# Kernel tuning notes

Hardware: AMD Instinct MI355X
Metric: run time of the kernel (lower is better)

Reference implementation:

```python
import math
import jax, jax.numpy as jnp
import numpy as np

LLM = 4096
QB = 512
SAM = 256
H = W = 64
OUT = 256
HEADS = 4
DH = SAM // HEADS
EPS = 1e-5


def _ln(x, g, b):
    mu = jnp.mean(x, axis=-1, keepdims=True)
    var = jnp.mean(jnp.square(x - mu), axis=-1, keepdims=True)
    return (x - mu) * jax.lax.rsqrt(var + EPS) * g + b


def _conv3x3(x, w):
    # x: (N,C,H,W), w: (O,I,3,3), padding=1
    return jax.lax.conv_general_dilated(
        x, w, window_strides=(1, 1), padding='SAME',
        dimension_numbers=('NCHW', 'OIHW', 'NCHW'))


def setup_inputs() -> dict:
    key = jax.random.key(0)
    ks = jax.random.split(key, 20)
    n = lambda k, sh, s: (jax.random.normal(k, sh, dtype=jnp.float32) * s)
    inp = {
        'image_embed': n(ks[0], (8, SAM, H, W), 1.0),
        'ref_vec': n(ks[1], (8, 32, LLM), 1.0),
        'querybook_slots': n(ks[2], (8, 32, QB), 1.0),
        # parameters (torch Linear layout: (out, in); conv: (O,I,kh,kw))
        'q_proj_w': n(ks[3], (HEADS * DH, LLM), 1.0 / math.sqrt(LLM)),
        'k_proj_w': n(ks[4], (HEADS * DH, SAM, 1, 1), 1.0 / math.sqrt(SAM)),
        'fuser_w1': n(ks[5], (HEADS, HEADS, 3, 3), 1.0 / math.sqrt(HEADS * 9)),
        'fuser_b1': n(ks[6], (HEADS,), 0.01),
        'fuser_w2': n(ks[7], (1, HEADS, 3, 3), 1.0 / math.sqrt(HEADS * 9)),
        'fuser_b2': jnp.full((1,), -1.8, dtype=jnp.float32),
        'qb_proj_w': n(ks[8], (LLM, QB), 1.0 / math.sqrt(QB)),
        'rf_ln_g': jnp.ones((2 * LLM,), jnp.float32),
        'rf_ln_b': jnp.zeros((2 * LLM,), jnp.float32),
        'rf_lin_w': n(ks[9], (LLM, 2 * LLM), 1.0 / math.sqrt(2 * LLM)),
        'rf_lin_b': n(ks[10], (LLM,), 0.01),
        'cf_ln_g': jnp.ones((LLM,), jnp.float32),
        'cf_ln_b': jnp.zeros((LLM,), jnp.float32),
        'cf_w1': n(ks[11], (LLM // 2, LLM), 1.0 / math.sqrt(LLM)),
        'cf_b1': n(ks[12], (LLM // 2,), 0.01),
        'cf_w2': n(ks[13], (1, LLM // 2), 1.0 / math.sqrt(LLM // 2)),
        'cf_b2': n(ks[14], (1,), 0.01),
    }
    return inp


def reference(image_embed, ref_vec, querybook_slots, q_proj_w, k_proj_w,
              fuser_w1, fuser_b1, fuser_w2, fuser_b2, qb_proj_w,
              rf_ln_g, rf_ln_b, rf_lin_w, rf_lin_b,
              cf_ln_g, cf_ln_b, cf_w1, cf_b1, cf_w2, cf_b2):
    B, C, h, w = image_embed.shape
    K = ref_vec.shape[1]
    # querybook projection + ref fuse
    qb = jnp.einsum('bkq,lq->bkl', querybook_slots, qb_proj_w)  # (B,K,LLM)
    cat = jnp.concatenate([ref_vec, qb], axis=-1)               # (B,K,2*LLM)
    fused = jax.nn.silu(jnp.einsum('bkc,lc->bkl', _ln(cat, rf_ln_g, rf_ln_b), rf_lin_w) + rf_lin_b)
    # per-slot query heads
    Q = jnp.einsum('bkl,ol->bko', fused, q_proj_w).reshape(B, K, HEADS, DH)
    # 1x1 conv key map -> (B,HEADS,DH,H,W)
    Kmap = jnp.einsum('bcxy,oc->boxy', image_embed, k_proj_w.reshape(HEADS * DH, SAM))
    Kmap = Kmap.reshape(B, HEADS, DH, h, w)
    # fused contraction over d_head (original materialized (B,K,HEADS,DH,H,W))
    logits_64_heads = jnp.einsum('bkhd,bhdxy->bkhxy', Q, Kmap) / math.sqrt(DH)
    x = logits_64_heads.reshape(B * K, HEADS, h, w)
    x = jax.nn.silu(_conv3x3(x, fuser_w1) + fuser_b1[None, :, None, None])
    logits_64 = _conv3x3(x, fuser_w2) + fuser_b2[None, :, None, None]  # (B*K,1,64,64)
    # bilinear upsample, align_corners=False (half-pixel centers)
    up = jax.image.resize(logits_64, (B * K, 1, OUT, OUT), method='bilinear')
    ref_logits_256 = up.reshape(B, K, OUT, OUT)
    # confidence head
    cfh = jax.nn.silu(jnp.einsum('bkl,ol->bko', _ln(fused, cf_ln_g, cf_ln_b), cf_w1) + cf_b1)
    conf_logits = (jnp.einsum('bko,lo->bkl', cfh, cf_w2) + cf_b2).squeeze(-1)  # (B,K)
    return ref_logits_256, conf_logits
```

## Files before the change

### kernel.cpp

```cpp
#include <hip/hip_runtime.h>

#define EPS 1e-5f

typedef __bf16 bf16_t;
typedef __bf16 bf16x8 __attribute__((ext_vector_type(8)));
typedef __bf16 bf16x4 __attribute__((ext_vector_type(4)));
typedef float f32x4 __attribute__((ext_vector_type(4)));

__device__ __forceinline__ float silu_f(float x) { return x / (1.f + __expf(-x)); }

__device__ __forceinline__ float block_sum(float v, float* tmp) {
#pragma unroll
  for (int off = 32; off > 0; off >>= 1) v += __shfl_down(v, off);
  __syncthreads();
  if ((threadIdx.x & 63) == 0) tmp[threadIdx.x >> 6] = v;
  __syncthreads();
  return tmp[0] + tmp[1] + tmp[2] + tmp[3];
}

__global__ __launch_bounds__(1024) void gemm_wide(
    const bf16_t* __restrict__ A, const float* __restrict__ B,
    bf16_t* __restrict__ Cpart, int N, int K, int KS) {
  __shared__ bf16_t As[2][256][72];
  __shared__ bf16_t Bs[2][128][72];
  const int t = threadIdx.x;
  const int lane = t & 63;
  const int w = t >> 6;
  const int n0 = blockIdx.x * 128;
  const int kbeg = blockIdx.y * KS;
  const int nt = KS >> 6;
  const int ar = t >> 2, ac = (t & 3) * 16;
  const int br = t >> 3, bc = (t & 7) * 8;
  const bf16_t* Ap = A + (size_t)ar * K + kbeg + ac;
  const float* Bp = B + (size_t)(n0 + br) * K + kbeg + bc;

  bf16x8 a0X, a1X, a0Y, a1Y, a0Z, a1Z;
  float4 b0X, b1X, b0Y, b1Y, b0Z, b1Z;

#define LOADSET(S, k0)                            \
  a0##S = *(const bf16x8*)(Ap + (k0));            \
  a1##S = *(const bf16x8*)(Ap + (k0) + 8);        \
  b0##S = *(const float4*)(Bp + (k0));            \
  b1##S = *(const float4*)(Bp + (k0) + 4);

#define STORESET(S, buf)                                                    \
  {                                                                         \
    *(bf16x8*)&As[buf][ar][ac] = a0##S;                                     \
    *(bf16x8*)&As[buf][ar][ac + 8] = a1##S;                                 \
    bf16x8 wv;                                                              \
    wv[0] = (bf16_t)b0##S.x; wv[1] = (bf16_t)b0##S.y;                       \
    wv[2] = (bf16_t)b0##S.z; wv[3] = (bf16_t)b0##S.w;                       \
    wv[4] = (bf16_t)b1##S.x; wv[5] = (bf16_t)b1##S.y;                       \
    wv[6] = (bf16_t)b1##S.z; wv[7] = (bf16_t)b1##S.w;                       \
    *(bf16x8*)&Bs[buf][br][bc] = wv;                                        \
  }

  f32x4 acc[4][2];
#pragma unroll
  for (int i = 0; i < 4; ++i)
#pragma unroll
    for (int j = 0; j < 2; ++j) acc[i][j] = f32x4{0.f, 0.f, 0.f, 0.f};

  const int wm = (w & 3) * 64;
  const int wn = (w >> 2) * 32;
  const int fr = lane & 15;
  const int kq = (lane >> 4) * 8;

  auto COMPUTE = [&](int buf) {
#pragma unroll
    for (int kk = 0; kk < 64; kk += 32) {
      bf16x8 af[4], bg[2];
#pragma unroll
      for (int i = 0; i < 4; ++i)
        af[i] = *(const bf16x8*)&As[buf][wm + 16 * i + fr][kk + kq];
#pragma unroll
      for (int j = 0; j < 2; ++j)
        bg[j] = *(const bf16x8*)&Bs[buf][wn + 16 * j + fr][kk + kq];
#pragma unroll
      for (int i = 0; i < 4; ++i)
#pragma unroll
        for (int j = 0; j < 2; ++j)
          acc[i][j] = __builtin_amdgcn_mfma_f32_16x16x32_bf16(af[i], bg[j], acc[i][j], 0, 0, 0);
    }
  };

#define SB __builtin_amdgcn_sched_barrier(0);
#define END_PHASE                                      \
  asm volatile("s_waitcnt lgkmcnt(0)" ::: "memory");   \
  SB __builtin_amdgcn_s_barrier(); SB

#define PHASE(s_, LS, SS, bufc)                              \
  if ((s_) < nt) {                                           \
    if ((s_) + 3 < nt) { LOADSET(LS, ((s_) + 3) * 64) }      \
    SB                                                       \
    if ((s_) + 1 < nt) { STORESET(SS, bufc ^ 1) }            \
    COMPUTE(bufc);                                           \
    END_PHASE                                                \
  }

  LOADSET(X, 0)
  if (1 < nt) { LOADSET(Y, 64) }
  if (2 < nt) { LOADSET(Z, 128) }
  SB
  STORESET(X, 0)
  END_PHASE

  for (int s6 = 0; s6 < nt; s6 += 6) {
    PHASE(s6 + 0, X, Y, 0)
    PHASE(s6 + 1, Y, Z, 1)
    PHASE(s6 + 2, Z, X, 0)
    PHASE(s6 + 3, X, Y, 1)
    PHASE(s6 + 4, Y, Z, 0)
    PHASE(s6 + 5, Z, X, 1)
  }
#undef LOADSET
#undef STORESET
#undef PHASE
#undef END_PHASE
#undef SB

  bf16_t* Cz = Cpart + (size_t)blockIdx.y * 256 * N;
  const int rh = (lane >> 4) * 4, col = lane & 15;
#pragma unroll
  for (int i = 0; i < 4; ++i)
#pragma unroll
    for (int j = 0; j < 2; ++j)
#pragma unroll
      for (int rr = 0; rr < 4; ++rr)
        Cz[(size_t)(wm + 16 * i + rh + rr) * N + n0 + wn + 16 * j + col] =
            (bf16_t)acc[i][j][rr];
}

__global__ __launch_bounds__(1024) void gemm_wide_s(
    const float* __restrict__ A, const float* __restrict__ B,
    bf16_t* __restrict__ Cpart, int N, int K, int KS) {
  __shared__ bf16_t As[256][72];
  __shared__ bf16_t Bs[128][72];
  const int t = threadIdx.x;
  const int lane = t & 63;
  const int w = t >> 6;
  const int n0 = blockIdx.x * 128;
  const int kbeg = blockIdx.y * KS;
  const int nt = KS >> 6;
  const int ar = t >> 2, ac = (t & 3) * 16;
  const int br = t >> 3, bc = (t & 7) * 8;
  const float* Ap = A + (size_t)ar * K + kbeg + ac;
  const float* Bp = B + (size_t)(n0 + br) * K + kbeg + bc;

  f32x4 acc[4][2];
#pragma unroll
  for (int i = 0; i < 4; ++i)
#pragma unroll
    for (int j = 0; j < 2; ++j) acc[i][j] = f32x4{0.f, 0.f, 0.f, 0.f};

  const int wm = (w & 3) * 64;
  const int wn = (w >> 2) * 32;
  const int fr = lane & 15;
  const int kq = (lane >> 4) * 8;

  for (int s = 0; s < nt; ++s) {
    float4 av[4], bv[2];
#pragma unroll
    for (int i = 0; i < 4; ++i) av[i] = *(const float4*)(Ap + s * 64 + 4 * i);
#pragma unroll
    for (int i = 0; i < 2; ++i) bv[i] = *(const float4*)(Bp + s * 64 + 4 * i);
    __syncthreads();
    {
      bf16x8 wa0, wa1, wb;
      wa0[0] = (bf16_t)av[0].x; wa0[1] = (bf16_t)av[0].y; wa0[2] = (bf16_t)av[0].z; wa0[3] = (bf16_t)av[0].w;
      wa0[4] = (bf16_t)av[1].x; wa0[5] = (bf16_t)av[1].y; wa0[6] = (bf16_t)av[1].z; wa0[7] = (bf16_t)av[1].w;
      wa1[0] = (bf16_t)av[2].x; wa1[1] = (bf16_t)av[2].y; wa1[2] = (bf16_t)av[2].z; wa1[3] = (bf16_t)av[2].w;
      wa1[4] = (bf16_t)av[3].x; wa1[5] = (bf16_t)av[3].y; wa1[6] = (bf16_t)av[3].z; wa1[7] = (bf16_t)av[3].w;
      wb[0] = (bf16_t)bv[0].x; wb[1] = (bf16_t)bv[0].y; wb[2] = (bf16_t)bv[0].z; wb[3] = (bf16_t)bv[0].w;
      wb[4] = (bf16_t)bv[1].x; wb[5] = (bf16_t)bv[1].y; wb[6] = (bf16_t)bv[1].z; wb[7] = (bf16_t)bv[1].w;
      *(bf16x8*)&As[ar][ac] = wa0;
      *(bf16x8*)&As[ar][ac + 8] = wa1;
      *(bf16x8*)&Bs[br][bc] = wb;
    }
    __syncthreads();
#pragma unroll
    for (int kk = 0; kk < 64; kk += 32) {
      bf16x8 af[4], bg[2];
#pragma unroll
      for (int i = 0; i < 4; ++i)
        af[i] = *(const bf16x8*)&As[wm + 16 * i + fr][kk + kq];
#pragma unroll
      for (int j = 0; j < 2; ++j)
        bg[j] = *(const bf16x8*)&Bs[wn + 16 * j + fr][kk + kq];
#pragma unroll
      for (int i = 0; i < 4; ++i)
#pragma unroll
        for (int j = 0; j < 2; ++j)
          acc[i][j] = __builtin_amdgcn_mfma_f32_16x16x32_bf16(af[i], bg[j], acc[i][j], 0, 0, 0);
    }
    __syncthreads();
  }

  bf16_t* Cz = Cpart + (size_t)blockIdx.y * 256 * N;
  const int rh = (lane >> 4) * 4, col = lane & 15;
#pragma unroll
  for (int i = 0; i < 4; ++i)
#pragma unroll
    for (int j = 0; j < 2; ++j)
#pragma unroll
      for (int rr = 0; rr < 4; ++rr)
        Cz[(size_t)(wm + 16 * i + rh + rr) * N + n0 + wn + 16 * j + col] =
            (bf16_t)acc[i][j][rr];
}

__global__ __launch_bounds__(256) void gemm_small(
    const bf16_t* __restrict__ A16, const float* __restrict__ B32, float* __restrict__ Cv,
    int M, int N, int K, int KS, int S) {
  __shared__ bf16_t As[64][72];
  __shared__ bf16_t Bs[64][72];
  const int t = threadIdx.x;
  const int lane = t & 63;
  const int w = t >> 6;
  const int s = blockIdx.z;
  const int n0 = blockIdx.x * 64;
  const int m0 = blockIdx.y * 64;
  const int kbeg = s * KS;

  f32x4 acc[2][2];
#pragma unroll
  for (int i = 0; i < 2; ++i)
#pragma unroll
    for (int j = 0; j < 2; ++j) acc[i][j] = f32x4{0.f, 0.f, 0.f, 0.f};

  const int wm = (w & 1) * 32, wn = (w >> 1) * 32;
  const int fr = lane & 15;
  const int kq = (lane >> 4) * 8;

  for (int k0 = kbeg; k0 < kbeg + KS; k0 += 64) {
    bf16x8 a8[2];
    float4 b4[4];
    {
      const int rr = t >> 2, c8 = (t & 3) * 8;
#pragma unroll
      for (int i = 0; i < 2; ++i)
        a8[i] = *(const bf16x8*)(A16 + (size_t)(m0 + rr) * K + k0 + c8 + 32 * i);
    }
    {
      const int rr = t >> 4, c4 = (t & 15) * 4;
#pragma unroll
      for (int i = 0; i < 4; ++i)
        b4[i] = *(const float4*)(B32 + (size_t)(n0 + rr + 16 * i) * K + k0 + c4);
    }
    __syncthreads();
    {
      const int rr = t >> 2, c8 = (t & 3) * 8;
#pragma unroll
      for (int i = 0; i < 2; ++i) *(bf16x8*)&As[rr][c8 + 32 * i] = a8[i];
    }
    {
      const int rr = t >> 4, c4 = (t & 15) * 4;
#pragma unroll
      for (int i = 0; i < 4; ++i) {
        bf16x4 v = {(bf16_t)b4[i].x, (bf16_t)b4[i].y, (bf16_t)b4[i].z, (bf16_t)b4[i].w};
        *(bf16x4*)&Bs[rr + 16 * i][c4] = v;
      }
    }
    __syncthreads();
#pragma unroll
    for (int kk = 0; kk < 64; kk += 32) {
      bf16x8 af[2], bg[2];
#pragma unroll
      for (int i = 0; i < 2; ++i) {
        af[i] = *(const bf16x8*)&As[wm + 16 * i + fr][kk + kq];
        bg[i] = *(const bf16x8*)&Bs[wn + 16 * i + fr][kk + kq];
      }
#pragma unroll
      for (int i = 0; i < 2; ++i)
#pragma unroll
        for (int j = 0; j < 2; ++j)
          acc[i][j] = __builtin_amdgcn_mfma_f32_16x16x32_bf16(af[i], bg[j], acc[i][j], 0, 0, 0);
    }
    __syncthreads();
  }

  const int rh = (lane >> 4) * 4;
  const int col = lane & 15;
#pragma unroll
  for (int i = 0; i < 2; ++i)
#pragma unroll
    for (int j = 0; j < 2; ++j)
#pragma unroll
      for (int rr = 0; rr < 4; ++rr)
        Cv[(size_t)s * M * N + (size_t)(m0 + wm + 16 * i + rh + rr) * N + n0 + wn + 16 * j + col] =
            acc[i][j][rr];
}

__global__ __launch_bounds__(512) void gemm_attn(
    const float* __restrict__ A, const float* __restrict__ B, bf16_t* __restrict__ C) {
  __shared__ bf16_t As[128][72];
  __shared__ bf16_t Bs[64][72];
  const int t = threadIdx.x;
  const int lane = t & 63;
  const int w = t >> 6;
  const int b = blockIdx.y;
  const int n0 = blockIdx.x * 64;
  const float* Ab = A + (size_t)b * 32768;
  const float* Bb = B + (size_t)b * 1048576;

  f32x4 acc[2][2];
#pragma unroll
  for (int i = 0; i < 2; ++i)
#pragma unroll
    for (int j = 0; j < 2; ++j) acc[i][j] = f32x4{0.f, 0.f, 0.f, 0.f};

  const int wm = (w & 3) * 32;
  const int wn = (w >> 2) * 32;
  const int fr = lane & 15;
  const int kq = (lane >> 4) * 8;

  for (int k0 = 0; k0 < 256; k0 += 64) {
    const int r = t >> 2, c4 = (t & 3) * 16;
    float4 a4[4];
#pragma unroll
    for (int i = 0; i < 4; ++i)
      a4[i] = *(const float4*)(Ab + (size_t)r * 256 + k0 + c4 + 4 * i);
    const int kr = t >> 3, nc = (t & 7) * 8;
    float4 b4[2];
#pragma unroll
    for (int i = 0; i < 2; ++i)
      b4[i] = *(const float4*)(Bb + (size_t)(k0 + kr) * 4096 + n0 + nc + 4 * i);
    __syncthreads();
#pragma unroll
    for (int i = 0; i < 4; ++i) {
      bf16x4 v = {(bf16_t)a4[i].x, (bf16_t)a4[i].y, (bf16_t)a4[i].z, (bf16_t)a4[i].w};
      *(bf16x4*)&As[r][c4 + 4 * i] = v;
    }
#pragma unroll
    for (int i = 0; i < 2; ++i) {
      Bs[nc + 4 * i + 0][kr] = (bf16_t)b4[i].x;
      Bs[nc + 4 * i + 1][kr] = (bf16_t)b4[i].y;
      Bs[nc + 4 * i + 2][kr] = (bf16_t)b4[i].z;
      Bs[nc + 4 * i + 3][kr] = (bf16_t)b4[i].w;
    }
    __syncthreads();
#pragma unroll
    for (int kk = 0; kk < 64; kk += 32) {
      bf16x8 af[2], bg[2];
#pragma unroll
      for (int i = 0; i < 2; ++i) {
        af[i] = *(const bf16x8*)&As[wm + 16 * i + fr][kk + kq];
        bg[i] = *(const bf16x8*)&Bs[wn + 16 * i + fr][kk + kq];
      }
#pragma unroll
      for (int i = 0; i < 2; ++i)
#pragma unroll
        for (int j = 0; j < 2; ++j)
          acc[i][j] = __builtin_amdgcn_mfma_f32_16x16x32_bf16(af[i], bg[j], acc[i][j], 0, 0, 0);
    }
    __syncthreads();
  }

  bf16_t* Cb = C + (size_t)b * 524288;
  const int rh = (lane >> 4) * 4, col = lane & 15;
#pragma unroll
  for (int i = 0; i < 2; ++i)
#pragma unroll
    for (int j = 0; j < 2; ++j)
#pragma unroll
      for (int rr = 0; rr < 4; ++rr)
        Cb[(size_t)(wm + 16 * i + rh + rr) * 4096 + n0 + wn + 16 * j + col] =
            (bf16_t)acc[i][j][rr];
}

template <int SILU_, int BIAS_>
__global__ __launch_bounds__(256) void reduce_b(
    const bf16_t* __restrict__ part, int S, long slice,
    const float* __restrict__ bias, float scale,
    float* __restrict__ outF, bf16_t* __restrict__ outB,
    long nmask, long total8) {
  long i8 = (long)blockIdx.x * 256 + threadIdx.x;
  if (i8 >= total8) return;
  long i = i8 * 8;
  float a[8] = {0.f, 0.f, 0.f, 0.f, 0.f, 0.f, 0.f, 0.f};
  for (int s = 0; s < S; ++s) {
    bf16x8 v = *(const bf16x8*)(part + (size_t)s * slice + i);
#pragma unroll
    for (int j = 0; j < 8; ++j) a[j] += (float)v[j];
  }
#pragma unroll
  for (int j = 0; j < 8; ++j) a[j] *= scale;
  if (BIAS_) {
    const float* bb = bias + (i & nmask);
#pragma unroll
    for (int j = 0; j < 8; ++j) a[j] += bb[j];
  }
  if (SILU_) {
#pragma unroll
    for (int j = 0; j < 8; ++j) a[j] = silu_f(a[j]);
  }
  if (outF) {
    float4 o0 = {a[0], a[1], a[2], a[3]}, o1 = {a[4], a[5], a[6], a[7]};
    *(float4*)(outF + i) = o0;
    *(float4*)(outF + i + 4) = o1;
  }
  if (outB) {
    bf16x8 o;
#pragma unroll
    for (int j = 0; j < 8; ++j) o[j] = (bf16_t)a[j];
    *(bf16x8*)(outB + i) = o;
  }
}

__global__ __launch_bounds__(256) void ln_fuse(
    const float* __restrict__ refv, const bf16_t* __restrict__ partQ, int S,
    const float* __restrict__ g, const float* __restrict__ bta, bf16_t* __restrict__ Y) {
  __shared__ float tmp[4];
  const int row = blockIdx.x;
  const int t = threadIdx.x;
  const long i0 = t * 16;
  float q[16];
#pragma unroll
  for (int j = 0; j < 16; ++j) q[j] = 0.f;
  for (int s = 0; s < S; ++s) {
    const bf16_t* p = partQ + (size_t)s * 1048576 + (size_t)row * 4096 + i0;
    bf16x8 v0 = *(const bf16x8*)(p);
    bf16x8 v1 = *(const bf16x8*)(p + 8);
#pragma unroll
    for (int j = 0; j < 8; ++j) { q[j] += (float)v0[j]; q[8 + j] += (float)v1[j]; }
  }
  const float* xr = refv + (size_t)row * 4096 + i0;
  float r[16];
#pragma unroll
  for (int j = 0; j < 4; ++j) {
    float4 v = *(const float4*)(xr + 4 * j);
    r[4 * j] = v.x; r[4 * j + 1] = v.y; r[4 * j + 2] = v.z; r[4 * j + 3] = v.w;
  }
  float s1 = 0.f, s2 = 0.f;
#pragma unroll
  for (int j = 0; j < 16; ++j) { s1 += r[j] + q[j]; s2 += r[j] * r[j] + q[j] * q[j]; }
  s1 = block_sum(s1, tmp);
  s2 = block_sum(s2, tmp);
  const float mu = s1 / 8192.f;
  const float inv = rsqrtf(s2 / 8192.f - mu * mu + EPS);
  bf16_t* y = Y + (size_t)row * 8192;
  bf16x8 o0, o1;
#pragma unroll
  for (int j = 0; j < 8; ++j) {
    o0[j] = (bf16_t)((r[j] - mu) * inv * g[i0 + j] + bta[i0 + j]);
    o1[j] = (bf16_t)((r[8 + j] - mu) * inv * g[i0 + 8 + j] + bta[i0 + 8 + j]);
  }
  *(bf16x8*)(y + i0) = o0;
  *(bf16x8*)(y + i0 + 8) = o1;
#pragma unroll
  for (int j = 0; j < 8; ++j) {
    o0[j] = (bf16_t)((q[j] - mu) * inv * g[4096 + i0 + j] + bta[4096 + i0 + j]);
    o1[j] = (bf16_t)((q[8 + j] - mu) * inv * g[4096 + i0 + 8 + j] + bta[4096 + i0 + 8 + j]);
  }
  *(bf16x8*)(y + 4096 + i0) = o0;
  *(bf16x8*)(y + 4096 + i0 + 8) = o1;
}

__global__ __launch_bounds__(256) void ln_rows(
    const float* __restrict__ X1, int L1,
    const float* __restrict__ g, const float* __restrict__ bta, bf16_t* __restrict__ Y) {
  __shared__ float tmp[4];
  const int row = blockIdx.x;
  const float* x1 = X1 + (size_t)row * L1;
  float s = 0.f, ss = 0.f;
  for (int i = threadIdx.x * 4; i < L1; i += 1024) {
    float4 v = *(const float4*)(x1 + i);
    s += v.x + v.y + v.z + v.w;
    ss += v.x * v.x + v.y * v.y + v.z * v.z + v.w * v.w;
  }
  s = block_sum(s, tmp);
  ss = block_sum(ss, tmp);
  const float mu = s / (float)L1;
  const float inv = rsqrtf(ss / (float)L1 - mu * mu + EPS);
  bf16_t* y = Y + (size_t)row * L1;
  for (int i = threadIdx.x * 4; i < L1; i += 1024) {
    float4 v = *(const float4*)(x1 + i);
    float4 gv = *(const float4*)(g + i);
    float4 bv = *(const float4*)(bta + i);
    bf16x4 o = {(bf16_t)((v.x - mu) * inv * gv.x + bv.x),
                (bf16_t)((v.y - mu) * inv * gv.y + bv.y),
                (bf16_t)((v.z - mu) * inv * gv.z + bv.z),
                (bf16_t)((v.w - mu) * inv * gv.w + bv.w)};
    *(bf16x4*)(y + i) = o;
  }
}

__global__ __launch_bounds__(256) void qw_fuse(
    const float* __restrict__ part8, const float* __restrict__ kW, float* __restrict__ QW) {
  __shared__ float q[256];
  const int bk = blockIdx.x;
  const int c = threadIdx.x;
  float sq = 0.f;
#pragma unroll
  for (int s = 0; s < 8; ++s) sq += part8[(size_t)s * 65536 + (size_t)bk * 256 + c];
  q[c] = 0.125f * sq;
  __syncthreads();
#pragma unroll
  for (int h = 0; h < 4; ++h) {
    float s = 0.f;
#pragma unroll 8
    for (int d = 0; d < 64; ++d)
      s += q[(h << 6) + d] * kW[(size_t)(((h << 6) + d) << 8) + c];
    QW[((size_t)(bk * 4 + h) << 8) + c] = s;
  }
}

__global__ __launch_bounds__(256) void conv_fused(
    const bf16_t* __restrict__ X, const float* __restrict__ W1,
    const float* __restrict__ B1, const float* __restrict__ W2,
    const float* __restrict__ B2, float* __restrict__ O) {
  __shared__ bf16_t lg[16384];
  __shared__ bf16_t mid[16384];
  __shared__ float lg64[4096];
  __shared__ float wsh[180];
  const int t = threadIdx.x;
  const size_t base = (size_t)blockIdx.x * 16384;
#pragma unroll
  for (int i = 0; i < 8; ++i) {
    int o = (i * 256 + t) * 8;
    *(bf16x8*)&lg[o] = *(const bf16x8*)(X + base + o);
  }
  if (t < 144) wsh[t] = W1[t];
  else if (t < 180) wsh[t] = W2[t - 144];
  __syncthreads();
  const int px0 = (t & 15) * 4, py0 = (t >> 4) * 4;
  {
    float acc1[4][16];
#pragma unroll
    for (int oc = 0; oc < 4; ++oc) {
      float bb = B1[oc];
#pragma unroll
      for (int p = 0; p < 16; ++p) acc1[oc][p] = bb;
    }
#pragma unroll
    for (int c = 0; c < 4; ++c) {
      float p[6][6];
#pragma unroll
      for (int yy = 0; yy < 6; ++yy) {
        int gy = py0 + yy - 1;
#pragma unroll
        for (int xx = 0; xx < 6; ++xx) {
          int gx = px0 + xx - 1;
          p[yy][xx] = ((unsigned)gy < 64u && (unsigned)gx < 64u)
                          ? (float)lg[c * 4096 + gy * 64 + gx] : 0.f;
        }
      }
#pragma unroll
      for (int oc = 0; oc < 4; ++oc) {
        float wr[9];
#pragma unroll
        for (int k = 0; k < 9; ++k) wr[k] = wsh[oc * 36 + c * 9 + k];
#pragma unroll
        for (int y = 0; y < 4; ++y)
#pragma unroll
          for (int x = 0; x < 4; ++x)
            acc1[oc][y * 4 + x] +=
                wr[0] * p[y][x] + wr[1] * p[y][x + 1] + wr[2] * p[y][x + 2]
              + wr[3] * p[y + 1][x] + wr[4] * p[y + 1][x + 1] + wr[5] * p[y + 1][x + 2]
              + wr[6] * p[y + 2][x] + wr[7] * p[y + 2][x + 1] + wr[8] * p[y + 2][x + 2];
      }
    }
#pragma unroll
    for (int oc = 0; oc < 4; ++oc)
#pragma unroll
      for (int y = 0; y < 4; ++y) {
        bf16x4 o;
#pragma unroll
        for (int x = 0; x < 4; ++x) o[x] = (bf16_t)silu_f(acc1[oc][y * 4 + x]);
        *(bf16x4*)&mid[oc * 4096 + (py0 + y) * 64 + px0] = o;
      }
  }
  __syncthreads();
  {
    float acc2[16];
    float bb = B2[0];
#pragma unroll
    for (int p = 0; p < 16; ++p) acc2[p] = bb;
#pragma unroll
    for (int c = 0; c < 4; ++c) {
      float p[6][6];
#pragma unroll
      for (int yy = 0; yy < 6; ++yy) {
        int gy = py0 + yy - 1;
#pragma unroll
        for (int xx = 0; xx < 6; ++xx) {
          int gx = px0 + xx - 1;
          p[yy][xx] = ((unsigned)gy < 64u && (unsigned)gx < 64u)
                          ? (float)mid[c * 4096 + gy * 64 + gx] : 0.f;
        }
      }
      float wr[9];
#pragma unroll
      for (int k = 0; k < 9; ++k) wr[k] = wsh[144 + c * 9 + k];
#pragma unroll
      for (int y = 0; y < 4; ++y)
#pragma unroll
        for (int x = 0; x < 4; ++x)
          acc2[y * 4 + x] +=
              wr[0] * p[y][x] + wr[1] * p[y][x + 1] + wr[2] * p[y][x + 2]
            + wr[3] * p[y + 1][x] + wr[4] * p[y + 1][x + 1] + wr[5] * p[y + 1][x + 2]
            + wr[6] * p[y + 2][x] + wr[7] * p[y + 2][x + 1] + wr[8] * p[y + 2][x + 2];
    }
#pragma unroll
    for (int y = 0; y < 4; ++y)
#pragma unroll
      for (int x = 0; x < 4; ++x) lg64[(py0 + y) * 64 + px0 + x] = acc2[y * 4 + x];
  }
  __syncthreads();
  float* Ob = O + (size_t)blockIdx.x * 65536;
  for (int rr = 0; rr < 64; ++rr) {
    int p4 = rr * 256 + t;
    int oy = p4 >> 6, ox0 = (p4 & 63) * 4;
    float sy = oy * 0.25f - 0.375f;
    int y0 = (int)floorf(sy);
    float wy = sy - (float)y0;
    int y1 = min(y0 + 1, 63); y0 = max(y0, 0);
    const float* r0 = &lg64[y0 * 64];
    const float* r1 = &lg64[y1 * 64];
    float4 o;
#pragma unroll
    for (int q = 0; q < 4; ++q) {
      int ox = ox0 + q;
      float sx = ox * 0.25f - 0.375f;
      int x0 = (int)floorf(sx);
      float wx = sx - (float)x0;
      int x1 = min(x0 + 1, 63); x0 = max(x0, 0);
      float v0 = r0[x0] + wx * (r0[x1] - r0[x0]);
      float v1 = r1[x0] + wx * (r1[x1] - r1[x0]);
      ((float*)&o)[q] = v0 + wy * (v1 - v0);
    }
    *(float4*)(Ob + oy * 256 + ox0) = o;
  }
}

__global__ __launch_bounds__(256) void conf_k(
    const float* __restrict__ cfh, const float* __restrict__ w2,
    const float* __restrict__ b2, float* __restrict__ out) {
  __shared__ float tmp[4];
  const int row = blockIdx.x;
  float s = 0.f;
  for (int i = threadIdx.x; i < 2048; i += 256)
    s += cfh[(size_t)row * 2048 + i] * w2[i];
  s = block_sum(s, tmp);
  if (threadIdx.x == 0) out[row] = s + b2[0];
}

extern "C" void kernel_launch(void* const* d_in, const int* in_sizes, int n_in,
                              void* d_out, int out_size, void* d_ws, size_t ws_size,
                              hipStream_t stream) {
  const float* img    = (const float*)d_in[0];
  const float* refv   = (const float*)d_in[1];
  const float* qs     = (const float*)d_in[2];
  const float* qpw    = (const float*)d_in[3];
  const float* kpw    = (const float*)d_in[4];
  const float* fw1    = (const float*)d_in[5];
  const float* fb1    = (const float*)d_in[6];
  const float* fw2    = (const float*)d_in[7];
  const float* fb2    = (const float*)d_in[8];
  const float* qbw    = (const float*)d_in[9];
  const float* rlg    = (const float*)d_in[10];
  const float* rlb    = (const float*)d_in[11];
  const float* rlw    = (const float*)d_in[12];
  const float* rlbias = (const float*)d_in[13];
  const float* clg    = (const float*)d_in[14];
  const float* clb    = (const float*)d_in[15];
  const float* cw1    = (const float*)d_in[16];
  const float* cb1    = (const float*)d_in[17];
  const float* cw2    = (const float*)d_in[18];
  const float* cb2    = (const float*)d_in[19];
  float* out = (float*)d_out;
  char* W = (char*)d_ws;

  bf16_t* partQ = (bf16_t*)(W + 0);
  bf16_t* partF = (bf16_t*)(W + 0);
  bf16_t* l64hb = (bf16_t*)(W + 0);
  bf16_t* partC = (bf16_t*)(W + 0);
  bf16_t* catln = (bf16_t*)(W + 16777216);
  float*  fus   = (float*)(W + 16777216);
  bf16_t* fusb  = (bf16_t*)(W + 20971520);
  bf16_t* lnf   = (bf16_t*)(W + 20971520);
  float*  part8 = (float*)(W + 23068672);
  float*  QW    = (float*)(W + 25165824);
  float*  cfh   = (float*)(W + 26214400);

  dim3 b256(256);

  gemm_wide_s<<<dim3(32, 8), dim3(1024), 0, stream>>>(qs, qbw, partQ, 4096, 512, 64);
  ln_fuse<<<dim3(256), b256, 0, stream>>>(refv, partQ, 8, rlg, rlb, catln);
  gemm_wide<<<dim3(32, 8), dim3(1024), 0, stream>>>(catln, rlw, partF, 4096, 8192, 1024);
  reduce_b<1, 1><<<dim3(512), b256, 0, stream>>>(
      partF, 8, 1048576L, rlbias, 1.f, fus, fusb, 4095L, 131072L);
  gemm_small<<<dim3(4, 4, 8), b256, 0, stream>>>(fusb, qpw, part8, 256, 256, 4096, 512, 8);
  qw_fuse<<<dim3(256), b256, 0, stream>>>(part8, kpw, QW);
  gemm_attn<<<dim3(64, 8), dim3(512), 0, stream>>>(QW, img, l64hb);
  conv_fused<<<dim3(256), b256, 0, stream>>>(l64hb, fw1, fb1, fw2, fb2, out);
  ln_rows<<<dim3(256), b256, 0, stream>>>(fus, 4096, clg, clb, lnf);
  gemm_wide<<<dim3(16, 16), dim3(1024), 0, stream>>>(lnf, cw1, partC, 2048, 4096, 256);
  reduce_b<1, 1><<<dim3(256), b256, 0, stream>>>(
      partC, 16, 524288L, cb1, 1.f, cfh, nullptr, 2047L, 65536L);
  conf_k<<<dim3(256), b256, 0, stream>>>(cfh, cw2, cb2, out + 16777216);
}
```

Baseline: 187.9 us.

## Load GEMM tiles directly into LDS with global_load_lds and swizzled layout

```diff
diff --git a/kernel.cpp b/kernel.cpp
--- a/kernel.cpp
+++ b/kernel.cpp
@@ -8,6 +8,12 @@
 typedef float f32x4 __attribute__((ext_vector_type(4)));
 
 __device__ __forceinline__ float silu_f(float x) { return x / (1.f + __expf(-x)); }
+
+__device__ __forceinline__ void gll16(const void* g, void* l) {
+  __builtin_amdgcn_global_load_lds(
+      (const __attribute__((address_space(1))) unsigned int*)g,
+      (__attribute__((address_space(3))) unsigned int*)l, 16, 0, 0);
+}
 
 __device__ __forceinline__ float block_sum(float v, float* tmp) {
 #pragma unroll
@@ -18,42 +24,28 @@
   return tmp[0] + tmp[1] + tmp[2] + tmp[3];
 }
 
-__global__ __launch_bounds__(1024) void gemm_wide(
+__global__ __launch_bounds__(1024) void gemm_gll(
     const bf16_t* __restrict__ A, const float* __restrict__ B,
     bf16_t* __restrict__ Cpart, int N, int K, int KS) {
-  __shared__ bf16_t As[2][256][72];
-  __shared__ bf16_t Bs[2][128][72];
+  __shared__ bf16_t AsL[2][16384];
+  __shared__ float BsL[2][8192];
   const int t = threadIdx.x;
   const int lane = t & 63;
   const int w = t >> 6;
   const int n0 = blockIdx.x * 128;
   const int kbeg = blockIdx.y * KS;
   const int nt = KS >> 6;
-  const int ar = t >> 2, ac = (t & 3) * 16;
-  const int br = t >> 3, bc = (t & 7) * 8;
-  const bf16_t* Ap = A + (size_t)ar * K + kbeg + ac;
-  const float* Bp = B + (size_t)(n0 + br) * K + kbeg + bc;
-
-  bf16x8 a0X, a1X, a0Y, a1Y, a0Z, a1Z;
-  float4 b0X, b1X, b0Y, b1Y, b0Z, b1Z;
-
-#define LOADSET(S, k0)                            \
-  a0##S = *(const bf16x8*)(Ap + (k0));            \
-  a1##S = *(const bf16x8*)(Ap + (k0) + 8);        \
-  b0##S = *(const float4*)(Bp + (k0));            \
-  b1##S = *(const float4*)(Bp + (k0) + 4);
-
-#define STORESET(S, buf)                                                    \
-  {                                                                         \
-    *(bf16x8*)&As[buf][ar][ac] = a0##S;                                     \
-    *(bf16x8*)&As[buf][ar][ac + 8] = a1##S;                                 \
-    bf16x8 wv;                                                              \
-    wv[0] = (bf16_t)b0##S.x; wv[1] = (bf16_t)b0##S.y;                       \
-    wv[2] = (bf16_t)b0##S.z; wv[3] = (bf16_t)b0##S.w;                       \
-    wv[4] = (bf16_t)b1##S.x; wv[5] = (bf16_t)b1##S.y;                       \
-    wv[6] = (bf16_t)b1##S.z; wv[7] = (bf16_t)b1##S.w;                       \
-    *(bf16x8*)&Bs[buf][br][bc] = wv;                                        \
-  }
+
+  const int arow0 = 16 * w + (lane >> 3);
+  const int adch = (lane & 7) ^ (lane >> 3);
+  const bf16_t* gA0 = A + (size_t)arow0 * K + kbeg + adch * 8;
+  const bf16_t* gA1 = gA0 + (size_t)8 * K;
+  const int brow0 = 8 * w + (lane >> 4);
+  const int brow1 = brow0 + 4;
+  const int bd0 = (lane & 15) ^ (brow0 & 15);
+  const int bd1 = (lane & 15) ^ (brow1 & 15);
+  const float* gB0 = B + (size_t)(n0 + brow0) * K + kbeg + bd0 * 4;
+  const float* gB1 = B + (size_t)(n0 + brow1) * K + kbeg + bd1 * 4;
 
   f32x4 acc[4][2];
 #pragma unroll
@@ -66,16 +58,44 @@
   const int fr = lane & 15;
   const int kq = (lane >> 4) * 8;
 
-  auto COMPUTE = [&](int buf) {
+  auto ISSUE = [&](int s, int p) {
+    const int koff = s * 64;
+    char* ab = (char*)&AsL[p][0] + 2 * w * 1024;
+    char* bb = (char*)&BsL[p][0] + 2 * w * 1024;
+    gll16(gA0 + koff, ab);
+    gll16(gA1 + koff, ab + 1024);
+    gll16(gB0 + koff, bb);
+    gll16(gB1 + koff, bb + 1024);
+  };
+
+  auto COMPUTE = [&](int p) {
+    const char* Ab = (const char*)&AsL[p][0];
+    const char* Bb = (const char*)&BsL[p][0];
 #pragma unroll
     for (int kk = 0; kk < 64; kk += 32) {
+      const int col = kk + kq;
       bf16x8 af[4], bg[2];
 #pragma unroll
-      for (int i = 0; i < 4; ++i)
-        af[i] = *(const bf16x8*)&As[buf][wm + 16 * i + fr][kk + kq];
-#pragma unroll
-      for (int j = 0; j < 2; ++j)
-        bg[j] = *(const bf16x8*)&Bs[buf][wn + 16 * j + fr][kk + kq];
+      for (int i = 0; i < 4; ++i) {
+        const int ra = wm + 16 * i + fr;
+        const int sa = (col >> 3) ^ (ra & 7);
+        af[i] = *(const bf16x8*)(Ab + ra * 128 + sa * 16);
+      }
+#pragma unroll
+      for (int j = 0; j < 2; ++j) {
+        const int rb = wn + 16 * j + fr;
+        const int c0 = col >> 2;
+        const int s0 = c0 ^ (rb & 15);
+        const int s1 = (c0 + 1) ^ (rb & 15);
+        f32x4 u0 = *(const f32x4*)(Bb + rb * 256 + s0 * 16);
+        f32x4 u1 = *(const f32x4*)(Bb + rb * 256 + s1 * 16);
+        bf16x8 bv;
+        bv[0] = (bf16_t)u0[0]; bv[1] = (bf16_t)u0[1];
+        bv[2] = (bf16_t)u0[2]; bv[3] = (bf16_t)u0[3];
+        bv[4] = (bf16_t)u1[0]; bv[5] = (bf16_t)u1[1];
+        bv[6] = (bf16_t)u1[2]; bv[7] = (bf16_t)u1[3];
+        bg[j] = bv;
+      }
 #pragma unroll
       for (int i = 0; i < 4; ++i)
 #pragma unroll
@@ -85,38 +105,24 @@
   };
 
 #define SB __builtin_amdgcn_sched_barrier(0);
-#define END_PHASE                                      \
-  asm volatile("s_waitcnt lgkmcnt(0)" ::: "memory");   \
-  SB __builtin_amdgcn_s_barrier(); SB
-
-#define PHASE(s_, LS, SS, bufc)                              \
-  if ((s_) < nt) {                                           \
-    if ((s_) + 3 < nt) { LOADSET(LS, ((s_) + 3) * 64) }      \
-    SB                                                       \
-    if ((s_) + 1 < nt) { STORESET(SS, bufc ^ 1) }            \
-    COMPUTE(bufc);                                           \
-    END_PHASE                                                \
-  }
-
-  LOADSET(X, 0)
-  if (1 < nt) { LOADSET(Y, 64) }
-  if (2 < nt) { LOADSET(Z, 128) }
-  SB
-  STORESET(X, 0)
-  END_PHASE
-
-  for (int s6 = 0; s6 < nt; s6 += 6) {
-    PHASE(s6 + 0, X, Y, 0)
-    PHASE(s6 + 1, Y, Z, 1)
-    PHASE(s6 + 2, Z, X, 0)
-    PHASE(s6 + 3, X, Y, 1)
-    PHASE(s6 + 4, Y, Z, 0)
-    PHASE(s6 + 5, Z, X, 1)
-  }
-#undef LOADSET
-#undef STORESET
-#undef PHASE
-#undef END_PHASE
+
+  ISSUE(0, 0);
+  if (nt > 1) ISSUE(1, 1);
+  for (int s = 0; s < nt; ++s) {
+    const int p = s & 1;
+    if (s + 1 < nt) {
+      asm volatile("s_waitcnt vmcnt(4)" ::: "memory");
+    } else {
+      asm volatile("s_waitcnt vmcnt(0)" ::: "memory");
+    }
+    SB __builtin_amdgcn_s_barrier(); SB
+    COMPUTE(p);
+    if (s + 2 < nt) {
+      asm volatile("s_waitcnt lgkmcnt(0)" ::: "memory");
+      SB __builtin_amdgcn_s_barrier(); SB
+      ISSUE(s + 2, p);
+    }
+  }
 #undef SB
 
   bf16_t* Cz = Cpart + (size_t)blockIdx.y * 256 * N;
@@ -686,7 +692,7 @@
 
   gemm_wide_s<<<dim3(32, 8), dim3(1024), 0, stream>>>(qs, qbw, partQ, 4096, 512, 64);
   ln_fuse<<<dim3(256), b256, 0, stream>>>(refv, partQ, 8, rlg, rlb, catln);
-  gemm_wide<<<dim3(32, 8), dim3(1024), 0, stream>>>(catln, rlw, partF, 4096, 8192, 1024);
+  gemm_gll<<<dim3(32, 8), dim3(1024), 0, stream>>>(catln, rlw, partF, 4096, 8192, 1024);
   reduce_b<1, 1><<<dim3(512), b256, 0, stream>>>(
       partF, 8, 1048576L, rlbias, 1.f, fus, fusb, 4095L, 131072L);
   gemm_small<<<dim3(4, 4, 8), b256, 0, stream>>>(fusb, qpw, part8, 256, 256, 4096, 512, 8);
@@ -694,8 +700,8 @@
   gemm_attn<<<dim3(64, 8), dim3(512), 0, stream>>>(QW, img, l64hb);
   conv_fused<<<dim3(256), b256, 0, stream>>>(l64hb, fw1, fb1, fw2, fb2, out);
   ln_rows<<<dim3(256), b256, 0, stream>>>(fus, 4096, clg, clb, lnf);
-  gemm_wide<<<dim3(16, 16), dim3(1024), 0, stream>>>(lnf, cw1, partC, 2048, 4096, 256);
+  gemm_gll<<<dim3(16, 8), dim3(1024), 0, stream>>>(lnf, cw1, partC, 2048, 4096, 512);
   reduce_b<1, 1><<<dim3(256), b256, 0, stream>>>(
-      partC, 16, 524288L, cb1, 1.f, cfh, nullptr, 2047L, 65536L);
+      partC, 8, 524288L, cb1, 1.f, cfh, nullptr, 2047L, 65536L);
   conf_k<<<dim3(256), b256, 0, stream>>>(cfh, cw2, cb2, out + 16777216);
 }
```

Result: no change. 184.7 us (-1.7%).
